# Performance work log

Measured on AMD Instinct MI355X. Metric: run time of the kernel, lower is better.

Reference implementation:

```python
import jax, jax.numpy as jnp
import numpy as np
import math

D_MODEL = 2048
N_HEADS = 16
HEAD_DIM = D_MODEL // N_HEADS


def setup_inputs() -> dict:
    key = jax.random.key(0)
    k1, k2, k3, k4 = jax.random.split(key, 4)
    bs, seq = 2, 2048
    x = jax.random.normal(k1, (bs, seq, D_MODEL), dtype=jnp.float32)
    # torch nn.Linear weights are [out, in]; y = x @ W.T
    scale_q = 1.0 / math.sqrt(D_MODEL)
    Wq = jax.random.uniform(k2, (D_MODEL, D_MODEL), jnp.float32, -scale_q, scale_q)
    Wkv = jax.random.uniform(k3, (2 * HEAD_DIM, D_MODEL), jnp.float32, -scale_q, scale_q)
    Wo = jax.random.uniform(k4, (D_MODEL, D_MODEL), jnp.float32, -scale_q, scale_q)
    return {"x": x, "Wq": Wq, "Wkv": Wkv, "Wo": Wo}


def reference(x, Wq, Wkv, Wo):
    bs, seq, _ = x.shape
    q = x @ Wq.T                      # [b, s, d_model]
    kv = x @ Wkv.T                    # [b, s, 2*head_dim]
    k, v = jnp.split(kv, 2, axis=-1)  # each [b, s, head_dim] (single shared KV head)
    q = q.reshape(bs, seq, N_HEADS, HEAD_DIM).transpose(0, 2, 1, 3)  # [b, h, s, d]
    # MQA: broadcast shared K/V across heads via einsum (no explicit expand)
    attn = jnp.einsum("bhqd,bkd->bhqk", q, k) / math.sqrt(HEAD_DIM)  # [b, h, s, s]
    causal = jnp.tril(jnp.ones((seq, seq), dtype=bool))
    attn = jnp.where(causal[None, None], attn, jnp.float32(-1e9))
    attn = jax.nn.softmax(attn, axis=-1)
    out = jnp.einsum("bhqk,bkd->bhqd", attn, v)                      # [b, h, s, d]
    out = out.transpose(0, 2, 1, 3).reshape(bs, seq, D_MODEL)
    return out @ Wo.T
```

## Files before the change

kernel.cpp:

```cpp
#include <hip/hip_runtime.h>
#include <hip/hip_bf16.h>

typedef __attribute__((ext_vector_type(8))) short bf16x8;
typedef __attribute__((ext_vector_type(4))) float f32x4;
typedef __attribute__((ext_vector_type(16))) float f32x16;
typedef __attribute__((ext_vector_type(4))) ushort u16x4;

#define AS1 __attribute__((address_space(1)))
#define AS3 __attribute__((address_space(3)))

static __device__ __forceinline__ ushort f2b(float f) {
    union { float f; unsigned u; } v;
    v.f = f;
    unsigned r = v.u + 0x7FFF + ((v.u >> 16) & 1);
    return (ushort)(r >> 16);
}

__global__ __launch_bounds__(256) void cvt_all(const float* __restrict__ x,
                                               const float* __restrict__ Wq,
                                               const float* __restrict__ Wkv,
                                               const float* __restrict__ Wo,
                                               ushort* __restrict__ xb,
                                               ushort* __restrict__ wqkvb,
                                               ushort* __restrict__ wob)
{
    int i = blockIdx.x * blockDim.x + threadIdx.x;
    const int stride = gridDim.x * blockDim.x;
    for (; i < 4325376; i += stride) {
        const float4* src; ushort4* dst; int j;
        if (i < 2097152)      { src = (const float4*)x;   dst = (ushort4*)xb;              j = i; }
        else if (i < 3145728) { src = (const float4*)Wq;  dst = (ushort4*)wqkvb;           j = i - 2097152; }
        else if (i < 3276800) { src = (const float4*)Wkv; dst = (ushort4*)wqkvb + 1048576; j = i - 3145728; }
        else                  { src = (const float4*)Wo;  dst = (ushort4*)wob;             j = i - 3276800; }
        float4 v = src[j];
        ushort4 o; o.x = f2b(v.x); o.y = f2b(v.y); o.z = f2b(v.z); o.w = f2b(v.w);
        dst[j] = o;
    }
}

template<bool F32OUT>
__global__ __launch_bounds__(256) void gemm_bt(const ushort* __restrict__ A,
                                               const ushort* __restrict__ B,
                                               void* __restrict__ Cv,
                                               int M, int N, int K)
{
    __shared__ ushort As[2][128 * 32];
    __shared__ ushort Bs[2][128 * 32];
    const int tid  = threadIdx.x;
    const int lane = tid & 63;
    const int wid  = tid >> 6;
    const int l15  = lane & 15;
    const int lg   = lane >> 4;
    const int nwg8 = gridDim.x >> 3;
    const int kblk = blockIdx.x;
    const int swz  = (kblk & 7) * nwg8 + (kblk >> 3);
    const int nx   = N >> 7;
    const int brow = (swz / nx) * 128;
    const int bcol = (swz % nx) * 128;
    const int wr = wid >> 1, wc = wid & 1;

    f32x4 acc[4][4] = {};

    auto stage = [&](int bi, int k0) {
        const ushort* Ap = A + (size_t)brow * K + k0;
        const ushort* Bp = B + (size_t)bcol * K + k0;
#pragma unroll
        for (int j = 0; j < 2; ++j) {
            const int ci = wid * 2 + j;
            const int G  = ci * 64 + lane;
            const int r  = G >> 2, gc = G & 3;
            const int sgc = gc ^ ((r >> 1) & 3);
            __builtin_amdgcn_global_load_lds(
                (const AS1 void*)(Ap + (size_t)r * K + sgc * 8),
                (AS3 void*)(&As[bi][ci * 512]), 16, 0, 0);
            __builtin_amdgcn_global_load_lds(
                (const AS1 void*)(Bp + (size_t)r * K + sgc * 8),
                (AS3 void*)(&Bs[bi][ci * 512]), 16, 0, 0);
        }
    };

    stage(0, 0);
    __syncthreads();
    int cur = 0;

    for (int k0 = 0; k0 < K; k0 += 32) {
        if (k0 + 32 < K) stage(cur ^ 1, k0 + 32);

        bf16x8 af[4], bfr[4];
#pragma unroll
        for (int m = 0; m < 4; ++m) {
            int row = wr * 64 + m * 16 + l15;
            int slot = lg ^ ((row >> 1) & 3);
            af[m] = *(const bf16x8*)(&As[cur][row * 32 + slot * 8]);
        }
#pragma unroll
        for (int n = 0; n < 4; ++n) {
            int row = wc * 64 + n * 16 + l15;
            int slot = lg ^ ((row >> 1) & 3);
            bfr[n] = *(const bf16x8*)(&Bs[cur][row * 32 + slot * 8]);
        }
#pragma unroll
        for (int m = 0; m < 4; ++m)
#pragma unroll
            for (int n = 0; n < 4; ++n)
                acc[m][n] = __builtin_amdgcn_mfma_f32_16x16x32_bf16(af[m], bfr[n], acc[m][n], 0, 0, 0);

        __syncthreads();
        cur ^= 1;
    }

#pragma unroll
    for (int m = 0; m < 4; ++m)
#pragma unroll
        for (int n = 0; n < 4; ++n) {
            int row0 = brow + wr * 64 + m * 16 + lg * 4;
            int col  = bcol + wc * 64 + n * 16 + l15;
#pragma unroll
            for (int j = 0; j < 4; ++j) {
                float v = acc[m][n][j];
                if (F32OUT)
                    ((float*)Cv)[(size_t)(row0 + j) * N + col] = v;
                else
                    ((ushort*)Cv)[(size_t)(row0 + j) * N + col] = f2b(v);
            }
        }
}

__global__ __launch_bounds__(256) void gemm_qkv(const ushort* __restrict__ A,
                                                const ushort* __restrict__ B,
                                                ushort* __restrict__ Cq,
                                                ushort* __restrict__ Ckv,
                                                ushort* __restrict__ Vt,
                                                int M, int K)
{
    __shared__ ushort As[2][128 * 32];
    __shared__ ushort Bs[2][128 * 32];
    const int tid  = threadIdx.x;
    const int lane = tid & 63;
    const int wid  = tid >> 6;
    const int l15  = lane & 15;
    const int lg   = lane >> 4;
    const int nwg8 = gridDim.x >> 3;
    const int kblk = blockIdx.x;
    const int swz  = (kblk & 7) * nwg8 + (kblk >> 3);
    const int brow = (swz / 18) * 128;
    const int bcol = (swz % 18) * 128;
    const int wr = wid >> 1, wc = wid & 1;

    f32x4 acc[4][4] = {};

    auto stage = [&](int bi, int k0) {
        const ushort* Ap = A + (size_t)brow * K + k0;
        const ushort* Bp = B + (size_t)bcol * K + k0;
#pragma unroll
        for (int j = 0; j < 2; ++j) {
            const int ci = wid * 2 + j;
            const int G  = ci * 64 + lane;
            const int r  = G >> 2, gc = G & 3;
            const int sgc = gc ^ ((r >> 1) & 3);
            __builtin_amdgcn_global_load_lds(
                (const AS1 void*)(Ap + (size_t)r * K + sgc * 8),
                (AS3 void*)(&As[bi][ci * 512]), 16, 0, 0);
            __builtin_amdgcn_global_load_lds(
                (const AS1 void*)(Bp + (size_t)r * K + sgc * 8),
                (AS3 void*)(&Bs[bi][ci * 512]), 16, 0, 0);
        }
    };

    stage(0, 0);
    __syncthreads();
    int cur = 0;

    for (int k0 = 0; k0 < K; k0 += 32) {
        if (k0 + 32 < K) stage(cur ^ 1, k0 + 32);

        bf16x8 af[4], bfr[4];
#pragma unroll
        for (int m = 0; m < 4; ++m) {
            int row = wr * 64 + m * 16 + l15;
            int slot = lg ^ ((row >> 1) & 3);
            af[m] = *(const bf16x8*)(&As[cur][row * 32 + slot * 8]);
        }
#pragma unroll
        for (int n = 0; n < 4; ++n) {
            int row = wc * 64 + n * 16 + l15;
            int slot = lg ^ ((row >> 1) & 3);
            bfr[n] = *(const bf16x8*)(&Bs[cur][row * 32 + slot * 8]);
        }
#pragma unroll
        for (int m = 0; m < 4; ++m)
#pragma unroll
            for (int n = 0; n < 4; ++n)
                acc[m][n] = __builtin_amdgcn_mfma_f32_16x16x32_bf16(af[m], bfr[n], acc[m][n], 0, 0, 0);

        __syncthreads();
        cur ^= 1;
    }

    const bool toK = (bcol == 2048);
    const bool toV = (bcol == 2176);
#pragma unroll
    for (int m = 0; m < 4; ++m)
#pragma unroll
        for (int n = 0; n < 4; ++n) {
            int row0 = brow + wr * 64 + m * 16 + lg * 4;
            int col  = bcol + wc * 64 + n * 16 + l15;
#pragma unroll
            for (int j = 0; j < 4; ++j) {
                float v = acc[m][n][j];
                int row = row0 + j;
                if (toV) {
                    int d = col - 2176;
                    int bb = row >> 11, s = row & 2047;
                    Vt[((size_t)(bb * 128 + d)) * 2048 + s] = f2b(v);
                } else if (toK) {
                    Ckv[(size_t)row * 256 + (col - 2048)] = f2b(v);
                } else {
                    Cq[(size_t)row * 2048 + col] = f2b(v);
                }
            }
        }
}

__global__ __launch_bounds__(256, 2) void mqa_attn12(const ushort* __restrict__ Q,
                                                     const ushort* __restrict__ KV,
                                                     const ushort* __restrict__ Vt,
                                                     ushort* __restrict__ O)
{
    const int tid = threadIdx.x, lane = tid & 63, wid = tid >> 6;
    const int c31 = lane & 31, H = lane >> 5;
    const int bid = blockIdx.x;
    const int a  = bid & 31;
    const int hp = (bid >> 5) & 7;
    const int b  = bid >> 8;
    const int h  = hp * 2 + (wid >> 1);
    const int p  = wid & 1;

    __shared__ __align__(16) ushort SMEM[32768];

    const ushort* KVb = KV + (size_t)b * 2048 * 256;
    const ushort* Vtb = Vt + (size_t)b * 128 * 2048;
    const float C2 = 0.12751763f;
    const float mC = 32.0f * C2;

    auto stageK = [&](int buf, int par, int t) {
        ushort* dst = SMEM + (buf * 2 + par) * 4096;
        const int kvb = t * 32;
#pragma unroll
        for (int i = 0; i < 8; ++i) {
            int G = i * 64 + lane;
            int r = G >> 4, gc = G & 15;
            int sgc = gc ^ (r & 15);
            __builtin_amdgcn_global_load_lds(
                (const AS1 void*)(KVb + (size_t)(kvb + r) * 256 + sgc * 8),
                (AS3 void*)(dst + i * 512), 16, 0, 0);
        }
    };
    auto stageV = [&](int buf, int par, int t) {
        ushort* dst = SMEM + 16384 + (buf * 2 + par) * 4096;
        const int kvb = t * 32;
#pragma unroll
        for (int i = 0; i < 8; ++i) {
            int G = i * 64 + lane;
            int g = G >> 3, s = G & 7;
            int u = s ^ (g & 7);
            int r = 2 * g + (u & 1);
            int cc = u >> 1;
            __builtin_amdgcn_global_load_lds(
                (const AS1 void*)(Vtb + (size_t)r * 2048 + kvb + cc * 8),
                (AS3 void*)(dst + G * 8), 16, 0, 0);
        }
    };

#pragma unroll 1
    for (int phase = 0; phase < 2; ++phase) {
        const int tile  = phase ? (63 - a) : a;
        const int qtile = tile * 32;
        const int U = tile + 1;
        const int S = (U + 1) >> 1;
        const size_t qrow = (size_t)(b * 2048 + qtile + c31);

        bf16x8 qf[8];
#pragma unroll
        for (int dk = 0; dk < 8; ++dk)
            qf[dk] = *(const bf16x8*)(Q + qrow * 2048 + h * 128 + dk * 16 + H * 8);

        float l_run = 0.f;
        f32x16 of[4];
#pragma unroll
        for (int dt = 0; dt < 4; ++dt)
#pragma unroll
            for (int r = 0; r < 16; ++r) of[dt][r] = 0.f;

        {
            int t = p;
            if (t < U) { if (wid < 2) stageK(0, p, t); else stageV(0, p, t); }
        }
        __syncthreads();

#pragma unroll 1
        for (int s = 0; s < S; ++s) {
            if (s + 1 < S) {
                int tn = 2 * (s + 1) + p;
                if (tn < U) { if (wid < 2) stageK((s + 1) & 1, p, tn); else stageV((s + 1) & 1, p, tn); }
            }
            const int t = 2 * s + p;
            if (t < U) {
                const ushort* Kb = SMEM + ((s & 1) * 2 + p) * 4096;
                const ushort* Vb = SMEM + 16384 + ((s & 1) * 2 + p) * 4096;
                const bool maskt = (t == tile);

                f32x16 sg = {0,0,0,0,0,0,0,0,0,0,0,0,0,0,0,0};
                __builtin_amdgcn_s_setprio(1);
#pragma unroll
                for (int dk = 0; dk < 8; ++dk) {
                    bf16x8 kf = *(const bf16x8*)(Kb + c31 * 128 + ((dk * 16 + H * 8) ^ ((c31 & 15) << 3)));
                    sg = __builtin_amdgcn_mfma_f32_32x32x16_bf16(kf, qf[dk], sg, 0, 0, 0);
                }
                __builtin_amdgcn_s_setprio(0);

                float e[16];
#pragma unroll
                for (int r = 0; r < 16; ++r) {
                    float v = sg[r];
                    if (maskt) {
                        int crow = (r & 3) + 8 * (r >> 2) + 4 * H;
                        if (crow > c31) v = -1e30f;
                    }
                    e[r] = __builtin_amdgcn_exp2f(__builtin_fmaf(v, C2, -mC));
                }
                float rsum = 0.f;
#pragma unroll
                for (int r = 0; r < 16; ++r) rsum += e[r];
                rsum += __shfl_xor(rsum, 32);
                l_run += rsum;

                unsigned pk[8];
#pragma unroll
                for (int i = 0; i < 8; ++i)
                    asm("v_cvt_pk_bf16_f32 %0, %1, %2" : "=v"(pk[i]) : "v"(e[2 * i]), "v"(e[2 * i + 1]));
                asm("v_permlane32_swap_b32 %0, %1" : "+v"(pk[0]), "+v"(pk[2]));
                asm("v_permlane32_swap_b32 %0, %1" : "+v"(pk[1]), "+v"(pk[3]));
                asm("v_permlane32_swap_b32 %0, %1" : "+v"(pk[4]), "+v"(pk[6]));
                asm("v_permlane32_swap_b32 %0, %1" : "+v"(pk[5]), "+v"(pk[7]));
                union { unsigned u[4]; bf16x8 v; } P0, P1;
                P0.u[0] = pk[0]; P0.u[1] = pk[1]; P0.u[2] = pk[2]; P0.u[3] = pk[3];
                P1.u[0] = pk[4]; P1.u[1] = pk[5]; P1.u[2] = pk[6]; P1.u[3] = pk[7];

                __builtin_amdgcn_s_setprio(1);
#pragma unroll
                for (int dt = 0; dt < 4; ++dt) {
                    int g  = dt * 16 + (c31 >> 1);
                    int sw = g & 7;
                    int b0 = c31 & 1;
                    int s0 = (2 * H + b0) ^ sw;
                    int s1 = (4 + 2 * H + b0) ^ sw;
                    bf16x8 v0 = *(const bf16x8*)(Vb + (g * 8 + s0) * 8);
                    bf16x8 v1 = *(const bf16x8*)(Vb + (g * 8 + s1) * 8);
                    of[dt] = __builtin_amdgcn_mfma_f32_32x32x16_bf16(v0, P0.v, of[dt], 0, 0, 0);
                    of[dt] = __builtin_amdgcn_mfma_f32_32x32x16_bf16(v1, P1.v, of[dt], 0, 0, 0);
                }
                __builtin_amdgcn_s_setprio(0);
            }
            __syncthreads();
        }

        float* mlb = (float*)SMEM;
        if (H == 0) mlb[wid * 32 + c31] = l_run;
        __syncthreads();
        {
            float lo = mlb[(wid ^ 1) * 32 + c31];
            float inv = 1.0f / (l_run + lo);
            float* ob = (float*)(SMEM + 512) + (wid >> 1) * 4096;
            if (p == 1) {
#pragma unroll
                for (int dt = 0; dt < 4; ++dt)
#pragma unroll
                    for (int rq = 0; rq < 4; ++rq) {
                        f32x4 w;
#pragma unroll
                        for (int j = 0; j < 4; ++j) w[j] = of[dt][rq * 4 + j];
                        *(f32x4*)(ob + ((dt * 4 + rq) * 64 + lane) * 4) = w;
                    }
            }
            __syncthreads();
            if (p == 0) {
                ushort* Orow = O + qrow * 2048 + h * 128;
#pragma unroll
                for (int dt = 0; dt < 4; ++dt)
#pragma unroll
                    for (int rq = 0; rq < 4; ++rq) {
                        f32x4 r4 = *(const f32x4*)(ob + ((dt * 4 + rq) * 64 + lane) * 4);
                        u16x4 o4;
#pragma unroll
                        for (int j = 0; j < 4; ++j)
                            o4[j] = f2b((of[dt][rq * 4 + j] + r4[j]) * inv);
                        int d0 = dt * 32 + rq * 8 + 4 * H;
                        *(u16x4*)(Orow + d0) = o4;
                    }
            }
        }
        __syncthreads();
    }
}

extern "C" void kernel_launch(void* const* d_in, const int* in_sizes, int n_in,
                              void* d_out, int out_size, void* d_ws, size_t ws_size,
                              hipStream_t stream) {
    const float* x   = (const float*)d_in[0];
    const float* Wq  = (const float*)d_in[1];
    const float* Wkv = (const float*)d_in[2];
    const float* Wo  = (const float*)d_in[3];

    char* ws = (char*)d_ws;
    ushort* xb    = (ushort*)(ws);
    ushort* wqkvb = (ushort*)(ws + 16777216);
    ushort* wob   = (ushort*)(ws + 35651584);
    ushort* qb    = (ushort*)(ws + 44040192);
    ushort* kvb   = (ushort*)(ws + 60817408);
    ushort* vtb   = (ushort*)(ws + 62914560);
    ushort* aob   = xb;

    cvt_all<<<2048, 256, 0, stream>>>(x, Wq, Wkv, Wo, xb, wqkvb, wob);

    gemm_qkv<<<576, 256, 0, stream>>>(xb, wqkvb, qb, kvb, vtb, 4096, 2048);
    mqa_attn12<<<512, 256, 0, stream>>>(qb, kvb, vtb, aob);
    gemm_bt<true><<<512, 256, 0, stream>>>(aob, wob, d_out, 4096, 2048, 2048);
}
```

Before: 175.4 us.

## Rewrite QKV GEMM as 256x256 tile, 8-wave kernel with quarter-staged pipeline

Replaces the 128x128 tile QKV projection GEMM with a 256x256 tile kernel using 512 threads (8 waves), K-step 64, and four sub-phases per K iteration. Each phase issues the loads for one 128-row half of A or B while computing one quadrant, using explicit vmcnt waits, barriers and s_setprio around the MFMA bursts. The aim is higher arithmetic intensity per byte loaded and better overlap of global-to-LDS transfers with compute. The cost is that only 144 workgroups are launched, which may underfill the GPU's compute units, and each thread holds a larger accumulator set, which raises register pressure.

```diff
diff --git a/kernel.cpp b/kernel.cpp
--- a/kernel.cpp
+++ b/kernel.cpp
@@ -126,100 +126,129 @@
         }
 }
 
-__global__ __launch_bounds__(256) void gemm_qkv(const ushort* __restrict__ A,
-                                                const ushort* __restrict__ B,
-                                                ushort* __restrict__ Cq,
-                                                ushort* __restrict__ Ckv,
-                                                ushort* __restrict__ Vt,
-                                                int M, int K)
+#define QKV_PHASE(MH, NH, STG) do {                                                      \
+    STG;                                                                                 \
+    if (NH == 0) {                                                                       \
+        _Pragma("unroll")                                                                \
+        for (int m = 0; m < 4; ++m) {                                                    \
+            _Pragma("unroll")                                                            \
+            for (int kh = 0; kh < 2; ++kh) {                                             \
+                int r  = MH * 128 + wr * 64 + m * 16 + l15;                              \
+                int sl = (kh * 4 + lg) ^ (r & 7);                                        \
+                af[m][kh] = *(const bf16x8*)(&Asm[cur][r * 64 + sl * 8]);                \
+            }                                                                            \
+        }                                                                                \
+    }                                                                                    \
+    _Pragma("unroll")                                                                    \
+    for (int n = 0; n < 2; ++n) {                                                        \
+        _Pragma("unroll")                                                                \
+        for (int kh = 0; kh < 2; ++kh) {                                                 \
+            int r  = NH * 128 + wc * 32 + n * 16 + l15;                                  \
+            int sl = (kh * 4 + lg) ^ (r & 7);                                            \
+            bf[n][kh] = *(const bf16x8*)(&Bsm[cur][r * 64 + sl * 8]);                    \
+        }                                                                                \
+    }                                                                                    \
+    __builtin_amdgcn_s_setprio(1);                                                       \
+    _Pragma("unroll")                                                                    \
+    for (int m = 0; m < 4; ++m) {                                                        \
+        _Pragma("unroll")                                                                \
+        for (int n = 0; n < 2; ++n) {                                                    \
+            acc[MH * 4 + m][NH * 2 + n] = __builtin_amdgcn_mfma_f32_16x16x32_bf16(       \
+                af[m][0], bf[n][0], acc[MH * 4 + m][NH * 2 + n], 0, 0, 0);               \
+            acc[MH * 4 + m][NH * 2 + n] = __builtin_amdgcn_mfma_f32_16x16x32_bf16(       \
+                af[m][1], bf[n][1], acc[MH * 4 + m][NH * 2 + n], 0, 0, 0);               \
+        }                                                                                \
+    }                                                                                    \
+    __builtin_amdgcn_s_setprio(0);                                                       \
+    asm volatile("s_waitcnt lgkmcnt(0)" ::: "memory");                                   \
+    asm volatile("s_waitcnt vmcnt(6)" ::: "memory");                                     \
+    __builtin_amdgcn_s_barrier();                                                        \
+} while (0)
+
+__global__ __launch_bounds__(512, 2) void gemm_qkv8(const ushort* __restrict__ A,
+                                                    const ushort* __restrict__ B,
+                                                    ushort* __restrict__ Cq,
+                                                    ushort* __restrict__ Ckv,
+                                                    ushort* __restrict__ Vt)
 {
-    __shared__ ushort As[2][128 * 32];
-    __shared__ ushort Bs[2][128 * 32];
+    constexpr int K  = 2048;
+    constexpr int NT = 32;
+    __shared__ ushort Asm[2][16384];
+    __shared__ ushort Bsm[2][16384];
+
     const int tid  = threadIdx.x;
     const int lane = tid & 63;
     const int wid  = tid >> 6;
     const int l15  = lane & 15;
     const int lg   = lane >> 4;
-    const int nwg8 = gridDim.x >> 3;
-    const int kblk = blockIdx.x;
-    const int swz  = (kblk & 7) * nwg8 + (kblk >> 3);
-    const int brow = (swz / 18) * 128;
-    const int bcol = (swz % 18) * 128;
-    const int wr = wid >> 1, wc = wid & 1;
-
-    f32x4 acc[4][4] = {};
-
-    auto stage = [&](int bi, int k0) {
-        const ushort* Ap = A + (size_t)brow * K + k0;
-        const ushort* Bp = B + (size_t)bcol * K + k0;
+    const int wr   = wid >> 2;
+    const int wc   = wid & 3;
+    const int bid  = blockIdx.x;
+    const int swz  = (bid & 7) * 18 + (bid >> 3);
+    const int brow = (swz / 9) * 256;
+    const int bcol = (swz % 9) * 256;
+
+    f32x4  acc[8][4] = {};
+    bf16x8 af[4][2], bf[2][2];
+
+    auto stageH = [&](int bi, int which, int t) {
+        const int k0 = t << 6;
+        const ushort* src;
+        ushort* dst;
+        if (which == 0)      { src = A + (size_t)brow * K + k0;         dst = &Asm[bi][0];    }
+        else if (which == 1) { src = A + (size_t)(brow + 128) * K + k0; dst = &Asm[bi][8192]; }
+        else if (which == 2) { src = B + (size_t)bcol * K + k0;         dst = &Bsm[bi][0];    }
+        else                 { src = B + (size_t)(bcol + 128) * K + k0; dst = &Bsm[bi][8192]; }
 #pragma unroll
         for (int j = 0; j < 2; ++j) {
-            const int ci = wid * 2 + j;
-            const int G  = ci * 64 + lane;
-            const int r  = G >> 2, gc = G & 3;
-            const int sgc = gc ^ ((r >> 1) & 3);
+            const int t8 = j * 512 + tid;
+            const int r  = t8 >> 3;
+            const int s  = (t8 & 7) ^ (r & 7);
             __builtin_amdgcn_global_load_lds(
-                (const AS1 void*)(Ap + (size_t)r * K + sgc * 8),
-                (AS3 void*)(&As[bi][ci * 512]), 16, 0, 0);
-            __builtin_amdgcn_global_load_lds(
-                (const AS1 void*)(Bp + (size_t)r * K + sgc * 8),
-                (AS3 void*)(&Bs[bi][ci * 512]), 16, 0, 0);
+                (const AS1 void*)(src + (size_t)r * K + s * 8),
+                (AS3 void*)(dst + (j * 512 + (wid << 6)) * 8), 16, 0, 0);
         }
     };
 
-    stage(0, 0);
-    __syncthreads();
-    int cur = 0;
-
-    for (int k0 = 0; k0 < K; k0 += 32) {
-        if (k0 + 32 < K) stage(cur ^ 1, k0 + 32);
-
-        bf16x8 af[4], bfr[4];
-#pragma unroll
-        for (int m = 0; m < 4; ++m) {
-            int row = wr * 64 + m * 16 + l15;
-            int slot = lg ^ ((row >> 1) & 3);
-            af[m] = *(const bf16x8*)(&As[cur][row * 32 + slot * 8]);
-        }
-#pragma unroll
-        for (int n = 0; n < 4; ++n) {
-            int row = wc * 64 + n * 16 + l15;
-            int slot = lg ^ ((row >> 1) & 3);
-            bfr[n] = *(const bf16x8*)(&Bs[cur][row * 32 + slot * 8]);
-        }
-#pragma unroll
-        for (int m = 0; m < 4; ++m)
-#pragma unroll
-            for (int n = 0; n < 4; ++n)
-                acc[m][n] = __builtin_amdgcn_mfma_f32_16x16x32_bf16(af[m], bfr[n], acc[m][n], 0, 0, 0);
-
-        __syncthreads();
-        cur ^= 1;
+    stageH(0, 0, 0); stageH(0, 1, 0); stageH(0, 2, 0); stageH(0, 3, 0);
+    stageH(1, 0, 1); stageH(1, 2, 1);
+    asm volatile("s_waitcnt vmcnt(6)" ::: "memory");
+    __builtin_amdgcn_s_barrier();
+
+#pragma unroll 1
+    for (int t = 0; t < NT; ++t) {
+        const int cur = t & 1;
+        const int nxt = cur ^ 1;
+        QKV_PHASE(0, 0, { if (t + 1 < NT) stageH(nxt, 1, t + 1); });
+        QKV_PHASE(0, 1, { if (t + 1 < NT) stageH(nxt, 3, t + 1); });
+        QKV_PHASE(1, 0, { if (t + 2 < NT) stageH(cur, 0, t + 2); });
+        QKV_PHASE(1, 1, { if (t + 2 < NT) stageH(cur, 2, t + 2); });
     }
 
-    const bool toK = (bcol == 2048);
-    const bool toV = (bcol == 2176);
+#pragma unroll
+    for (int MH = 0; MH < 2; ++MH)
 #pragma unroll
     for (int m = 0; m < 4; ++m)
 #pragma unroll
-        for (int n = 0; n < 4; ++n) {
-            int row0 = brow + wr * 64 + m * 16 + lg * 4;
-            int col  = bcol + wc * 64 + n * 16 + l15;
-#pragma unroll
-            for (int j = 0; j < 4; ++j) {
-                float v = acc[m][n][j];
-                int row = row0 + j;
-                if (toV) {
-                    int d = col - 2176;
-                    int bb = row >> 11, s = row & 2047;
-                    Vt[((size_t)(bb * 128 + d)) * 2048 + s] = f2b(v);
-                } else if (toK) {
-                    Ckv[(size_t)row * 256 + (col - 2048)] = f2b(v);
-                } else {
-                    Cq[(size_t)row * 2048 + col] = f2b(v);
-                }
-            }
-        }
+    for (int NH = 0; NH < 2; ++NH)
+#pragma unroll
+    for (int n = 0; n < 2; ++n) {
+        const int row0 = brow + MH * 128 + wr * 64 + m * 16 + lg * 4;
+        const int col  = bcol + NH * 128 + wc * 32 + n * 16 + l15;
+        const f32x4 v4 = acc[MH * 4 + m][NH * 2 + n];
+#pragma unroll
+        for (int j = 0; j < 4; ++j) {
+            const float v = v4[j];
+            const int row = row0 + j;
+            if (col < 2048) {
+                Cq[(size_t)row * 2048 + col] = f2b(v);
+            } else if (col < 2176) {
+                Ckv[(size_t)row * 256 + (col - 2048)] = f2b(v);
+            } else {
+                Vt[((size_t)((row >> 11) * 128 + (col - 2176))) * 2048 + (row & 2047)] = f2b(v);
+            }
+        }
+    }
 }
 
 __global__ __launch_bounds__(256, 2) void mqa_attn12(const ushort* __restrict__ Q,
@@ -423,7 +452,7 @@
 
     cvt_all<<<2048, 256, 0, stream>>>(x, Wq, Wkv, Wo, xb, wqkvb, wob);
 
-    gemm_qkv<<<576, 256, 0, stream>>>(xb, wqkvb, qb, kvb, vtb, 4096, 2048);
+    gemm_qkv8<<<144, 512, 0, stream>>>(xb, wqkvb, qb, kvb, vtb);
     mqa_attn12<<<512, 256, 0, stream>>>(qb, kvb, vtb, aob);
     gemm_bt<true><<<512, 256, 0, stream>>>(aob, wob, d_out, 4096, 2048, 2048);
 }
```

Result: slower. 203.5 us (+16.0%).
